# Kernel optimization log

Measured on AMD Instinct MI355X. Metric: run time of the kernel, lower is better.

The kernel has to match this reference:

```python
import jax, jax.numpy as jnp
import numpy as np

B, T, C, K, L = 32, 4096, 8, 64, 100000
EPS = 1e-12


def _fit_quantile_edges(flat):
    # flat: [L, C] numpy. Faithful to GroupTokenizer._fit_quantile (vectorized over channels).
    idx = np.floor(np.arange(K + 1) * (L - 1) / K).astype(np.int64)
    idx = np.clip(idx, None, L - 1)
    vals = np.sort(flat, axis=0)            # [L, C] sorted per channel
    l = vals[idx[:K]].T.copy()              # [C, K]; l[:,0] = vals[idx[0]] = min
    r = vals[idx[1:]].T.copy()              # [C, K]
    l[:, 0] = vals[0]                       # mn
    r[:, -1] = vals[-1]                     # mx
    return l.astype(np.float32), r.astype(np.float32)


def setup_inputs() -> dict:
    key = jax.random.key(0)
    k1, _ = jax.random.split(key)
    rng = np.random.default_rng(0)
    flat = rng.normal(size=(L, C)).astype(np.float32)
    l, r = _fit_quantile_edges(flat)
    y = jax.random.normal(k1, (B, T, C), dtype=jnp.float32)
    return {"y": y, "left_edges": jnp.asarray(l), "right_edges": jnp.asarray(r)}


def reference(y, left_edges, right_edges):
    # y: [B, T, C]; edges: [C, K]
    k = left_edges.shape[-1]
    yk = y[..., None]                                   # [B,T,C,1]
    in_bin = (yk >= left_edges) & (yk < right_edges)    # [B,T,C,K]
    has_bin = in_bin.any(axis=-1)                       # [B,T,C]
    labels = jnp.argmax(in_bin, axis=-1)                # [B,T,C]
    labels = jnp.where(has_bin, labels, k - 1)
    cidx = jnp.arange(left_edges.shape[0])              # [C]
    left_sel = left_edges[cidx, labels]                 # [B,T,C]
    right_sel = right_edges[cidx, labels]               # [B,T,C]
    width = jnp.maximum(right_sel - left_sel, EPS)
    delta = jnp.clip((y - left_sel) / width, 0.0, 1.0)  # [B,T,C]
    onehot = labels[..., None] == jnp.arange(k)         # [B,T,C,K]
    reg = jnp.where(onehot, delta[..., None], jnp.asarray(-1.0, y.dtype))
    return labels, reg
```

## Files before the change

### kernel.cpp

```cpp
#include <hip/hip_runtime.h>

#define N_ELEM (32 * 4096 * 8)
#define CCH 8
#define KB 64
#define GPW 2
#define WPB 4

typedef float vfloat4 __attribute__((ext_vector_type(4)));

__global__ __launch_bounds__(256) void group_tokenizer_kernel(
    const float* __restrict__ y,
    const float* __restrict__ le,
    const float* __restrict__ re,
    float* __restrict__ out,
    int ngroups) {
  __shared__ float ls[CCH][KB + 1];
  __shared__ float rs[CCH][KB + 1];
  const int tid = threadIdx.x;
  for (int t = tid; t < CCH * KB; t += blockDim.x) {
    ls[t >> 6][t & 63] = le[t];
    rs[t >> 6][t & 63] = re[t];
  }
  __syncthreads();

  const int lane = tid & 63;
  const int wid = tid >> 6;
  const int g0 = (blockIdx.x * WPB + wid) * GPW;
  if (g0 >= ngroups) return;

  const int c = lane & (CCH - 1);
  const float* lr = ls[c];
  const float* rr = rs[c];

  int labelA[GPW];
  float deltaA[GPW];
#pragma unroll
  for (int t = 0; t < GPW; ++t) {
    const int g = g0 + t;
    const float yv = (g < ngroups) ? y[g * 64 + lane] : 0.0f;

    int lo = 0, hi = KB;
#pragma unroll
    for (int it = 0; it < 7; ++it) {
      const int mid = (lo + hi) >> 1;
      const bool cond = yv < rr[mid];
      hi = cond ? mid : hi;
      lo = cond ? lo : mid + 1;
    }
    const int label = (lo < KB && yv >= lr[lo]) ? lo : (KB - 1);
    const float left = lr[label];
    const float width = fmaxf(rr[label] - left, 1e-12f);
    labelA[t] = label;
    deltaA[t] = fminf(fmaxf((yv - left) / width, 0.0f), 1.0f);
  }

#pragma unroll
  for (int t = 0; t < GPW; ++t) {
    const int g = g0 + t;
    if (g < ngroups) out[g * 64 + lane] = (float)labelA[t];
  }

  const int kst = (lane & 15) << 2;
#pragma unroll
  for (int t = 0; t < GPW; ++t) {
    const int g = g0 + t;
    if (g >= ngroups) break;
    vfloat4* regv = (vfloat4*)(out + (size_t)N_ELEM + (size_t)g * (64 * KB));
    const int label = labelA[t];
    const float delta = deltaA[t];
#pragma unroll
    for (int j = 0; j < 16; ++j) {
      const int src = (j << 2) + (lane >> 4);
      const int lbl = __shfl(label, src, 64);
      const float dlt = __shfl(delta, src, 64);
      vfloat4 v;
      v.x = (kst + 0 == lbl) ? dlt : -1.0f;
      v.y = (kst + 1 == lbl) ? dlt : -1.0f;
      v.z = (kst + 2 == lbl) ? dlt : -1.0f;
      v.w = (kst + 3 == lbl) ? dlt : -1.0f;
      regv[(j << 6) + lane] = v;
    }
  }
}

extern "C" void kernel_launch(void* const* d_in, const int* in_sizes, int n_in,
                              void* d_out, int out_size, void* d_ws, size_t ws_size,
                              hipStream_t stream) {
  const float* y = (const float*)d_in[0];
  const float* le = (const float*)d_in[1];
  const float* re = (const float*)d_in[2];
  float* out = (float*)d_out;

  const int n = in_sizes[0];
  const int ngroups = n / 64;
  const int gpb = WPB * GPW;
  const int blocks = (ngroups + gpb - 1) / gpb;

  group_tokenizer_kernel<<<blocks, 256, 0, stream>>>(y, le, re, out, ngroups);
}
```

Measured before the change: 266.5 us.

## Split tokenizer into search kernel and grid-stride one-hot sweep kernel

Splits the fused kernel into two. The first runs a per-element binary search that writes labels to the output and deltas to workspace. The second is a grid-stride sweep that builds the one-hot regression tensor from those stored labels and deltas with vector4 stores. The aim is to decouple the output-write-bound sweep from the search and drop the cross-lane shuffles, at the cost of an extra launch and an extra round trip of labels and deltas through global memory. The original fused kernel is kept as a fallback for when no workspace is available.

```diff
diff --git a/kernel.cpp b/kernel.cpp
--- a/kernel.cpp
+++ b/kernel.cpp
@@ -3,12 +3,74 @@
 #define N_ELEM (32 * 4096 * 8)
 #define CCH 8
 #define KB 64
-#define GPW 2
-#define WPB 4
 
 typedef float vfloat4 __attribute__((ext_vector_type(4)));
 
-__global__ __launch_bounds__(256) void group_tokenizer_kernel(
+__global__ __launch_bounds__(256) void search_kernel(
+    const float* __restrict__ y,
+    const float* __restrict__ le,
+    const float* __restrict__ re,
+    float* __restrict__ labels_out,
+    float* __restrict__ deltas_out,
+    int nelem) {
+  __shared__ float ls[CCH][KB + 1];
+  __shared__ float rs[CCH][KB + 1];
+  const int tid = threadIdx.x;
+  for (int t = tid; t < CCH * KB; t += blockDim.x) {
+    ls[t >> 6][t & 63] = le[t];
+    rs[t >> 6][t & 63] = re[t];
+  }
+  __syncthreads();
+
+  const int stride = gridDim.x * blockDim.x;
+  for (int e = blockIdx.x * blockDim.x + tid; e < nelem; e += stride) {
+    const float yv = y[e];
+    const int c = e & (CCH - 1);
+    const float* lr = ls[c];
+    const float* rr = rs[c];
+
+    int lo = 0, hi = KB;
+#pragma unroll
+    for (int it = 0; it < 7; ++it) {
+      const int mid = (lo + hi) >> 1;
+      const bool cond = yv < rr[mid];
+      hi = cond ? mid : hi;
+      lo = cond ? lo : mid + 1;
+    }
+    const int label = (lo < KB && yv >= lr[lo]) ? lo : (KB - 1);
+    const float left = lr[label];
+    const float width = fmaxf(rr[label] - left, 1e-12f);
+    const float delta = fminf(fmaxf((yv - left) / width, 0.0f), 1.0f);
+
+    labels_out[e] = (float)label;
+    deltas_out[e] = delta;
+  }
+}
+
+__global__ __launch_bounds__(256) void compose_sweep_kernel(
+    const float* __restrict__ labels,
+    const float* __restrict__ deltas,
+    float* __restrict__ reg,
+    long nvec4) {
+  vfloat4* v = (vfloat4*)reg;
+  const long stride = (long)gridDim.x * blockDim.x;
+  for (long i = (long)blockIdx.x * blockDim.x + threadIdx.x; i < nvec4; i += stride) {
+    const int e = (int)(i >> 4);
+    const int k0 = ((int)i & 15) << 2;
+    const int lbl = (int)labels[e];
+    const float dlt = deltas[e];
+    vfloat4 v4;
+    v4.x = (k0 + 0 == lbl) ? dlt : -1.0f;
+    v4.y = (k0 + 1 == lbl) ? dlt : -1.0f;
+    v4.z = (k0 + 2 == lbl) ? dlt : -1.0f;
+    v4.w = (k0 + 3 == lbl) ? dlt : -1.0f;
+    v[i] = v4;
+  }
+}
+
+#define GPW 2
+#define WPB 4
+__global__ __launch_bounds__(256) void group_tokenizer_fallback(
     const float* __restrict__ y,
     const float* __restrict__ le,
     const float* __restrict__ re,
@@ -38,7 +100,6 @@
   for (int t = 0; t < GPW; ++t) {
     const int g = g0 + t;
     const float yv = (g < ngroups) ? y[g * 64 + lane] : 0.0f;
-
     int lo = 0, hi = KB;
 #pragma unroll
     for (int it = 0; it < 7; ++it) {
@@ -93,8 +154,16 @@
 
   const int n = in_sizes[0];
   const int ngroups = n / 64;
-  const int gpb = WPB * GPW;
-  const int blocks = (ngroups + gpb - 1) / gpb;
 
-  group_tokenizer_kernel<<<blocks, 256, 0, stream>>>(y, le, re, out, ngroups);
+  if (d_ws != nullptr && ws_size >= (size_t)n * sizeof(float)) {
+    float* deltas = (float*)d_ws;
+    search_kernel<<<2048, 256, 0, stream>>>(y, le, re, out, deltas, n);
+    const long nvec4 = (long)n * KB / 4;
+    compose_sweep_kernel<<<1024, 256, 0, stream>>>(out, deltas, out + (size_t)N_ELEM,
+                                                   nvec4);
+  } else {
+    const int gpb = WPB * GPW;
+    const int blocks = (ngroups + gpb - 1) / gpb;
+    group_tokenizer_fallback<<<blocks, 256, 0, stream>>>(y, le, re, out, ngroups);
+  }
 }
```

After: 272.6 us. 1.02x slower.
